# Kernel tuning notes

Measured on AMD Instinct MI355X. Metric: run time of the kernel, lower is better.

## Reference

```python
import jax, jax.numpy as jnp
import numpy as np

INPUT_DIM = 1024
OUTPUT_DIM = 1024
DEGREE = 8
BATCH = 8192


def setup_inputs() -> dict:
    key = jax.random.key(0)
    k1, k2 = jax.random.split(key)
    x = jax.random.normal(k1, (BATCH, INPUT_DIM), dtype=jnp.float32)
    std = 1.0 / (INPUT_DIM * (DEGREE + 1))
    cheby_coeffs = jax.random.normal(k2, (DEGREE + 1, INPUT_DIM, OUTPUT_DIM), dtype=jnp.float32) * std
    tanh_scale = jnp.array(1.0, dtype=jnp.float32)
    tanh_bias = jnp.array(0.0, dtype=jnp.float32)
    return {"x": x, "cheby_coeffs": cheby_coeffs, "tanh_scale": tanh_scale, "tanh_bias": tanh_bias}


def _cheby_basis(x, degree):
    Ts = [jnp.ones_like(x)]
    if degree >= 1:
        Ts.append(x)
    for _ in range(2, degree + 1):
        Ts.append(2.0 * x * Ts[-1] - Ts[-2])
    return jnp.stack(Ts, axis=0)


def reference(x, cheby_coeffs, tanh_scale, tanh_bias):
    degree = cheby_coeffs.shape[0] - 1
    input_dim = cheby_coeffs.shape[1]
    xf = x.reshape(-1, input_dim)
    xt = jnp.tanh(xf * tanh_scale + tanh_bias)            # (B, I)
    cheby = _cheby_basis(xt, degree)                       # (D+1, B, I)
    # bmm over degree then sum over degree == single contraction
    y = jnp.einsum('dbi,dio->bo', cheby, cheby_coeffs)     # (B, O)
    return y
```

## Files before the change

### kernel.cpp

```cpp
#include <hip/hip_runtime.h>
#include <hip/hip_bf16.h>

typedef __attribute__((ext_vector_type(8))) short short8;
typedef __attribute__((ext_vector_type(4))) float f32x4;
typedef __attribute__((ext_vector_type(16))) float f32x16;

#define WS_B0_OFFSET  18874368u

__global__ void wt2_kernel(const float* __restrict__ W, short* __restrict__ Wt2) {
    int bid = blockIdx.x;
    int d = bid >> 7, q = bid & 127;
    int t = threadIdx.x;
    const float* src = W + (size_t)d * 1048576 + (size_t)q * 8 * 1024;
    short* dst = Wt2 + ((size_t)(d * 128 + q) << 13);
#pragma unroll
    for (int u = 0; u < 4; u++) {
        int o = u * 256 + t;
        short8 v;
#pragma unroll
        for (int j = 0; j < 8; j++)
            v[j] = (short)__bfloat16_as_ushort(__float2bfloat16(src[(size_t)j * 1024 + o]));
        *(short8*)(dst + (size_t)o * 8) = v;
    }
}

__global__ void colsum1(const float* __restrict__ W, float* __restrict__ part) {
    int s = blockIdx.x >> 2;
    int o = (blockIdx.x & 3) * 256 + threadIdx.x;
    const float* p = W + (size_t)s * 32 * 1024 + o;
    float acc = 0.f;
#pragma unroll
    for (int i = 0; i < 32; i++) acc += p[(size_t)i * 1024];
    part[s * 1024 + o] = acc;
}
__global__ void colsum2(const float* __restrict__ part, float* __restrict__ b0) {
    int o = blockIdx.x * 256 + threadIdx.x;
    float acc = 0.f;
#pragma unroll
    for (int s = 0; s < 32; s++) acc += part[s * 1024 + o];
    b0[o] = acc;
}

__device__ __forceinline__ float fast_tanh(float t) {
    float e = __expf(t + t);
    return 1.0f - 2.0f * __builtin_amdgcn_rcpf(e + 1.0f);
}

extern "C" __global__ void __launch_bounds__(512, 2)
cheby_gemm(const float* __restrict__ x, const short* __restrict__ Wt2,
           const float* __restrict__ b0v, const float* __restrict__ scp,
           const float* __restrict__ bip, float* __restrict__ out) {
    __shared__ __align__(16) char lds[49152];

    const int tid = threadIdx.x, lane = tid & 63, wid = tid >> 6;
    const int wc = wid & 3, kh = wid >> 2;
    const int tn = blockIdx.x & 3, tm = blockIdx.x >> 2;
    const int m0 = tm << 7, n0 = tn << 8;
    const float sc = scp[0], bi = bip[0];
    const char* wtb = (const char*)Wt2;

    const int arow = tid >> 2, ac = tid & 3;
    const int wbyte0 = ac * 2048 + ((arow ^ (ac << 1)) << 4);
    const float* xptr = x + (size_t)(m0 + arow) * 1024 + ac * 8;

    const int cfr = kh * 2 + (lane >> 5);
    const int abase = cfr * 2048 + (((lane & 31) ^ (cfr << 1)) << 4);
    int bofs[2];
#pragma unroll
    for (int n = 0; n < 2; n++)
        bofs[n] = cfr * 16384 + (n0 + wc * 64 + n * 32 + (lane & 31)) * 16;

    auto bld = [&](short8* bf, int dd, int icc) {
        const char* p = wtb + ((size_t)(dd * 128 + icc * 4) << 14);
#pragma unroll
        for (int n = 0; n < 2; n++)
            bf[n] = *(const short8*)(p + bofs[n]);
    };

    f32x4 xv0, xv1;
    auto loadx = [&](int icc) {
        const float* p = xptr + (icc << 5);
        xv0 = *(const f32x4*)p;
        xv1 = *(const f32x4*)(p + 4);
    };

    float x2[8], tA[8], tB[8];
    auto dotanh = [&]() {
#pragma unroll
        for (int j = 0; j < 4; j++) {
            tA[j]     = fast_tanh(fmaf(xv0[j], sc, bi));
            tA[j + 4] = fast_tanh(fmaf(xv1[j], sc, bi));
        }
#pragma unroll
        for (int j = 0; j < 8; j++) x2[j] = tA[j] + tA[j];
    };
    auto writeA = [&](const float* t, int wbuf) {
        short8 v;
#pragma unroll
        for (int j = 0; j < 8; j++)
            v[j] = (short)__bfloat16_as_ushort(__float2bfloat16(t[j]));
        *(short8*)(lds + wbuf * 8192 + wbyte0) = v;
    };
    auto readA = [&](short8* af, int buf) {
#pragma unroll
        for (int m = 0; m < 4; m++)
            af[m] = *(const short8*)(lds + buf * 8192 + abase + m * 512);
    };

    f32x16 acc[4][2];
#pragma unroll
    for (int n = 0; n < 2; n++) {
        float v = (kh == 0) ? b0v[n0 + wc * 64 + n * 32 + (lane & 31)] : 0.0f;
        f32x16 a;
#pragma unroll
        for (int r = 0; r < 16; r++) a[r] = v;
#pragma unroll
        for (int m = 0; m < 4; m++) acc[m][n] = a;
    }

    auto domfma = [&](const short8* af, const short8* bf) {
        __builtin_amdgcn_s_setprio(1);
#pragma unroll
        for (int m = 0; m < 4; m++)
#pragma unroll
            for (int n = 0; n < 2; n++)
                acc[m][n] = __builtin_amdgcn_mfma_f32_32x32x16_bf16(af[m], bf[n], acc[m][n], 0, 0, 0);
        __builtin_amdgcn_s_setprio(0);
    };

    short8 af0[4], af1[4], bfA[2], bfB[2];

#define DRAIN_BAR                                                 \
    __builtin_amdgcn_sched_barrier(0);                            \
    asm volatile("s_waitcnt lgkmcnt(0)" ::: "memory");            \
    __builtin_amdgcn_s_barrier();

    loadx(0);
    bld(bfA, 1, 0);
    dotanh();
    writeA(tA, 0);
    DRAIN_BAR
    readA(af0, 0);
    __builtin_amdgcn_sched_barrier(0);

#define RSTEP(AFU, AFP, BFU, BFL, LD, LIC, WB, RECUR, XPRE)       \
    {                                                             \
        domfma(AFU, BFU);                                         \
        __builtin_amdgcn_sched_barrier(0);                        \
        bld(BFL, LD, LIC);                                        \
        if (XPRE) loadx(icn);                                     \
        RECUR                                                     \
        DRAIN_BAR                                                 \
        readA(AFP, WB);                                           \
        __builtin_amdgcn_sched_barrier(0);                        \
    }
#define REC_T2  { for (int j = 0; j < 8; j++) tB[j] = fmaf(x2[j], tA[j], -1.0f);  writeA(tB, 1); }
#define REC_BA(WB) { for (int j = 0; j < 8; j++) tA[j] = fmaf(x2[j], tB[j], -tA[j]); writeA(tA, WB); }
#define REC_AB(WB) { for (int j = 0; j < 8; j++) tB[j] = fmaf(x2[j], tA[j], -tB[j]); writeA(tB, WB); }
#define REC_TANH { dotanh(); writeA(tA, 0); }

    for (int ic = 0; ic < 32; ++ic) {
        const int icn = ic < 31 ? ic + 1 : 31;
        RSTEP(af0, af1, bfA, bfB, 2, ic, 1, REC_T2,     0)
        RSTEP(af1, af0, bfB, bfA, 3, ic, 0, REC_BA(0),  0)
        RSTEP(af0, af1, bfA, bfB, 4, ic, 1, REC_AB(1),  0)
        RSTEP(af1, af0, bfB, bfA, 5, ic, 0, REC_BA(0),  0)
        RSTEP(af0, af1, bfA, bfB, 6, ic, 1, REC_AB(1),  0)
        RSTEP(af1, af0, bfB, bfA, 7, ic, 0, REC_BA(0),  1)
        RSTEP(af0, af1, bfA, bfB, 8, ic, 1, REC_AB(1),  0)
        RSTEP(af1, af0, bfB, bfA, 1, icn, 0, REC_TANH,  0)
    }
#undef RSTEP
#undef DRAIN_BAR

#pragma unroll
    for (int m = 0; m < 4; m++) {
        if (kh == 1) {
#pragma unroll
            for (int n = 0; n < 2; n++) {
                char* base = lds + 16384 + (wc * 2 + n) * 4096 + lane * 64;
#pragma unroll
                for (int q = 0; q < 4; q++) {
                    f32x4 v = {acc[m][n][q * 4 + 0], acc[m][n][q * 4 + 1],
                               acc[m][n][q * 4 + 2], acc[m][n][q * 4 + 3]};
                    *(f32x4*)(base + ((q ^ (lane & 3)) << 4)) = v;
                }
            }
        }
        __syncthreads();
        if (kh == 0) {
#pragma unroll
            for (int n = 0; n < 2; n++) {
                const char* base = lds + 16384 + (wc * 2 + n) * 4096 + lane * 64;
#pragma unroll
                for (int q = 0; q < 4; q++) {
                    f32x4 v = *(const f32x4*)(base + ((q ^ (lane & 3)) << 4));
#pragma unroll
                    for (int e = 0; e < 4; e++) acc[m][n][q * 4 + e] += v[e];
                }
            }
        }
        __syncthreads();
    }

    if (kh == 0) {
#pragma unroll
        for (int m = 0; m < 4; m++) {
            int rbase = m0 + m * 32 + ((lane >> 5) << 2);
#pragma unroll
            for (int n = 0; n < 2; n++) {
                int colg = n0 + wc * 64 + n * 32 + (lane & 31);
#pragma unroll
                for (int r = 0; r < 16; r++) {
                    int rowg = rbase + (r & 3) + 8 * (r >> 2);
                    out[(size_t)rowg * 1024 + colg] = acc[m][n][r];
                }
            }
        }
    }
}

extern "C" void kernel_launch(void* const* d_in, const int* in_sizes, int n_in,
                              void* d_out, int out_size, void* d_ws, size_t ws_size,
                              hipStream_t stream) {
    const float* x  = (const float*)d_in[0];
    const float* W  = (const float*)d_in[1];
    const float* sc = (const float*)d_in[2];
    const float* bi = (const float*)d_in[3];
    float* out = (float*)d_out;

    short* Wt2 = (short*)d_ws;
    float* b0  = (float*)((char*)d_ws + WS_B0_OFFSET);
    float* part = out;

    hipLaunchKernelGGL(wt2_kernel, dim3(9 * 128), dim3(256), 0, stream, W, Wt2);
    hipLaunchKernelGGL(colsum1, dim3(128), dim3(256), 0, stream, W, part);
    hipLaunchKernelGGL(colsum2, dim3(4), dim3(256), 0, stream, part, b0);
    hipLaunchKernelGGL(cheby_gemm, dim3(256), dim3(512), 0, stream, x, Wt2, b0, sc, bi, out);
}
```

Measured before the change: 166.9 us.

## Process two Chebyshev degrees per barrier region with four-buffer LDS ring

Restructures the main loop so each barrier-separated region handles two degrees: it reads two A tiles from LDS, issues two MFMA bursts, prefetches two B fragments and computes two recurrence steps before a single barrier. The LDS A buffer grows from two to four slots (48KB to 64KB total) and the reduction scratch moves up accordingly. This halves the number of workgroup barriers and lgkm drains per K chunk. The cost is more live registers (four B fragment sets plus two A sets) and more LDS, which may pressure the two-blocks-per-CU occupancy target.

```diff
diff --git a/kernel.cpp b/kernel.cpp
--- a/kernel.cpp
+++ b/kernel.cpp
@@ -50,7 +50,7 @@
 cheby_gemm(const float* __restrict__ x, const short* __restrict__ Wt2,
            const float* __restrict__ b0v, const float* __restrict__ scp,
            const float* __restrict__ bip, float* __restrict__ out) {
-    __shared__ __align__(16) char lds[49152];
+    __shared__ __align__(16) char lds[65536];
 
     const int tid = threadIdx.x, lane = tid & 63, wid = tid >> 6;
     const int wc = wid & 3, kh = wid >> 2;
@@ -101,11 +101,6 @@
             v[j] = (short)__bfloat16_as_ushort(__float2bfloat16(t[j]));
         *(short8*)(lds + wbuf * 8192 + wbyte0) = v;
     };
-    auto readA = [&](short8* af, int buf) {
-#pragma unroll
-        for (int m = 0; m < 4; m++)
-            af[m] = *(const short8*)(lds + buf * 8192 + abase + m * 512);
-    };
 
     f32x16 acc[4][2];
 #pragma unroll
@@ -118,7 +113,7 @@
         for (int m = 0; m < 4; m++) acc[m][n] = a;
     }
 
-    auto domfma = [&](const short8* af, const short8* bf) {
+    auto burst = [&](const short8* af, const short8* bf) {
         __builtin_amdgcn_s_setprio(1);
 #pragma unroll
         for (int m = 0; m < 4; m++)
@@ -128,49 +123,66 @@
         __builtin_amdgcn_s_setprio(0);
     };
 
-    short8 af0[4], af1[4], bfA[2], bfB[2];
+    short8 bf0[2], bf1[2], bf2[2], bf3[2];
 
 #define DRAIN_BAR                                                 \
     __builtin_amdgcn_sched_barrier(0);                            \
     asm volatile("s_waitcnt lgkmcnt(0)" ::: "memory");            \
-    __builtin_amdgcn_s_barrier();
+    __builtin_amdgcn_s_barrier();                                 \
+    __builtin_amdgcn_sched_barrier(0);
+
+#define REGION(RA, RB, BU0, BU1, BL0, BL1, LD0, LD1, LIC, XPRE, RECUR)  \
+    {                                                                   \
+        short8 afa[4], afb[4];                                          \
+_Pragma("unroll")                                                       \
+        for (int m = 0; m < 4; m++)                                     \
+            afa[m] = *(const short8*)(lds + (RA) * 8192 + abase + m * 512); \
+        burst(afa, BU0);                                                \
+_Pragma("unroll")                                                       \
+        for (int m = 0; m < 4; m++)                                     \
+            afb[m] = *(const short8*)(lds + (RB) * 8192 + abase + m * 512); \
+        burst(afb, BU1);                                                \
+        bld(BL0, LD0, LIC); bld(BL1, LD1, LIC);                         \
+        if (XPRE) loadx(icn);                                           \
+        RECUR                                                           \
+        DRAIN_BAR                                                       \
+    }
+#define REC_STD(WA, WB)                                                 \
+    {                                                                   \
+_Pragma("unroll")                                                       \
+        for (int j = 0; j < 8; j++) tA[j] = fmaf(x2[j], tB[j], -tA[j]); \
+        writeA(tA, WA);                                                 \
+_Pragma("unroll")                                                       \
+        for (int j = 0; j < 8; j++) tB[j] = fmaf(x2[j], tA[j], -tB[j]); \
+        writeA(tB, WB);                                                 \
+    }
+#define REC_TANH(WA, WB)                                                \
+    {                                                                   \
+        dotanh();                                                       \
+_Pragma("unroll")                                                       \
+        for (int j = 0; j < 8; j++) tB[j] = fmaf(x2[j], tA[j], -1.0f);  \
+        writeA(tA, WA);                                                 \
+        writeA(tB, WB);                                                 \
+    }
 
     loadx(0);
-    bld(bfA, 1, 0);
+    bld(bf0, 1, 0); bld(bf1, 2, 0);
     dotanh();
-    writeA(tA, 0);
+#pragma unroll
+    for (int j = 0; j < 8; j++) tB[j] = fmaf(x2[j], tA[j], -1.0f);
+    writeA(tA, 1); writeA(tB, 2);
     DRAIN_BAR
-    readA(af0, 0);
-    __builtin_amdgcn_sched_barrier(0);
-
-#define RSTEP(AFU, AFP, BFU, BFL, LD, LIC, WB, RECUR, XPRE)       \
-    {                                                             \
-        domfma(AFU, BFU);                                         \
-        __builtin_amdgcn_sched_barrier(0);                        \
-        bld(BFL, LD, LIC);                                        \
-        if (XPRE) loadx(icn);                                     \
-        RECUR                                                     \
-        DRAIN_BAR                                                 \
-        readA(AFP, WB);                                           \
-        __builtin_amdgcn_sched_barrier(0);                        \
-    }
-#define REC_T2  { for (int j = 0; j < 8; j++) tB[j] = fmaf(x2[j], tA[j], -1.0f);  writeA(tB, 1); }
-#define REC_BA(WB) { for (int j = 0; j < 8; j++) tA[j] = fmaf(x2[j], tB[j], -tA[j]); writeA(tA, WB); }
-#define REC_AB(WB) { for (int j = 0; j < 8; j++) tB[j] = fmaf(x2[j], tA[j], -tB[j]); writeA(tB, WB); }
-#define REC_TANH { dotanh(); writeA(tA, 0); }
 
     for (int ic = 0; ic < 32; ++ic) {
         const int icn = ic < 31 ? ic + 1 : 31;
-        RSTEP(af0, af1, bfA, bfB, 2, ic, 1, REC_T2,     0)
-        RSTEP(af1, af0, bfB, bfA, 3, ic, 0, REC_BA(0),  0)
-        RSTEP(af0, af1, bfA, bfB, 4, ic, 1, REC_AB(1),  0)
-        RSTEP(af1, af0, bfB, bfA, 5, ic, 0, REC_BA(0),  0)
-        RSTEP(af0, af1, bfA, bfB, 6, ic, 1, REC_AB(1),  0)
-        RSTEP(af1, af0, bfB, bfA, 7, ic, 0, REC_BA(0),  1)
-        RSTEP(af0, af1, bfA, bfB, 8, ic, 1, REC_AB(1),  0)
-        RSTEP(af1, af0, bfB, bfA, 1, icn, 0, REC_TANH,  0)
-    }
-#undef RSTEP
+        REGION(1, 2, bf0, bf1, bf2, bf3, 3, 4, ic,  0, REC_STD(3, 0))
+        REGION(3, 0, bf2, bf3, bf0, bf1, 5, 6, ic,  0, REC_STD(1, 2))
+        REGION(1, 2, bf0, bf1, bf2, bf3, 7, 8, ic,  1, REC_STD(3, 0))
+        REGION(3, 0, bf2, bf3, bf0, bf1, 1, 2, icn, 0, REC_TANH(1, 2))
+    }
+#undef REGION
+#undef REC_STD
+#undef REC_TANH
 #undef DRAIN_BAR
 
 #pragma unroll
@@ -178,7 +190,7 @@
         if (kh == 1) {
 #pragma unroll
             for (int n = 0; n < 2; n++) {
-                char* base = lds + 16384 + (wc * 2 + n) * 4096 + lane * 64;
+                char* base = lds + 32768 + (wc * 2 + n) * 4096 + lane * 64;
 #pragma unroll
                 for (int q = 0; q < 4; q++) {
                     f32x4 v = {acc[m][n][q * 4 + 0], acc[m][n][q * 4 + 1],
@@ -191,7 +203,7 @@
         if (kh == 0) {
 #pragma unroll
             for (int n = 0; n < 2; n++) {
-                const char* base = lds + 16384 + (wc * 2 + n) * 4096 + lane * 64;
+                const char* base = lds + 32768 + (wc * 2 + n) * 4096 + lane * 64;
 #pragma unroll
                 for (int q = 0; q < 4; q++) {
                     f32x4 v = *(const f32x4*)(base + ((q ^ (lane & 3)) << 4));
```

Result: faster. 151.2 us (-9.4%).

## Reshape warp tile to 64x128 and move A reads into each step

Applied to the files above, without the earlier changes.

Warps within each K-half now form a 2x2 grid, each owning a 64-row by 128-column tile, where before each owned the full 128 rows by 64 columns. This halves the A-fragment LDS reads per warp and doubles the global B fragment loads per warp, so shared-memory traffic goes down while global/L2 load volume goes up. The per-step schedule is also reordered: A fragments are read from LDS at the start of each step alongside the next B prefetch, then the MFMA burst runs before the barrier. This removes the separate af0/af1 double-buffer registers, but each step's MFMAs now wait on their own LDS reads.

```diff
diff --git a/kernel.cpp b/kernel.cpp
--- a/kernel.cpp
+++ b/kernel.cpp
@@ -53,7 +53,7 @@
     __shared__ __align__(16) char lds[49152];
 
     const int tid = threadIdx.x, lane = tid & 63, wid = tid >> 6;
-    const int wc = wid & 3, kh = wid >> 2;
+    const int wr = wid & 1, wc = (wid >> 1) & 1, kh = wid >> 2;
     const int tn = blockIdx.x & 3, tm = blockIdx.x >> 2;
     const int m0 = tm << 7, n0 = tn << 8;
     const float sc = scp[0], bi = bip[0];
@@ -64,16 +64,16 @@
     const float* xptr = x + (size_t)(m0 + arow) * 1024 + ac * 8;
 
     const int cfr = kh * 2 + (lane >> 5);
-    const int abase = cfr * 2048 + (((lane & 31) ^ (cfr << 1)) << 4);
-    int bofs[2];
-#pragma unroll
-    for (int n = 0; n < 2; n++)
-        bofs[n] = cfr * 16384 + (n0 + wc * 64 + n * 32 + (lane & 31)) * 16;
+    const int abase = cfr * 2048 + (((lane & 31) ^ (cfr << 1)) << 4) + wr * 1024;
+    int bofs[4];
+#pragma unroll
+    for (int n = 0; n < 4; n++)
+        bofs[n] = (cfr << 14) + ((n0 + wc * 128 + n * 32 + (lane & 31)) << 4);
 
     auto bld = [&](short8* bf, int dd, int icc) {
         const char* p = wtb + ((size_t)(dd * 128 + icc * 4) << 14);
 #pragma unroll
-        for (int n = 0; n < 2; n++)
+        for (int n = 0; n < 4; n++)
             bf[n] = *(const short8*)(p + bofs[n]);
     };
 
@@ -101,119 +101,122 @@
             v[j] = (short)__bfloat16_as_ushort(__float2bfloat16(t[j]));
         *(short8*)(lds + wbuf * 8192 + wbyte0) = v;
     };
-    auto readA = [&](short8* af, int buf) {
-#pragma unroll
-        for (int m = 0; m < 4; m++)
-            af[m] = *(const short8*)(lds + buf * 8192 + abase + m * 512);
-    };
-
-    f32x16 acc[4][2];
-#pragma unroll
-    for (int n = 0; n < 2; n++) {
-        float v = (kh == 0) ? b0v[n0 + wc * 64 + n * 32 + (lane & 31)] : 0.0f;
+
+    f32x16 acc[2][4];
+#pragma unroll
+    for (int n = 0; n < 4; n++) {
+        float v = (kh == 0) ? b0v[n0 + wc * 128 + n * 32 + (lane & 31)] : 0.0f;
         f32x16 a;
 #pragma unroll
         for (int r = 0; r < 16; r++) a[r] = v;
-#pragma unroll
-        for (int m = 0; m < 4; m++) acc[m][n] = a;
-    }
-
-    auto domfma = [&](const short8* af, const short8* bf) {
+        acc[0][n] = a;
+        acc[1][n] = a;
+    }
+
+    auto burst = [&](const short8* af, const short8* bf) {
         __builtin_amdgcn_s_setprio(1);
 #pragma unroll
-        for (int m = 0; m < 4; m++)
-#pragma unroll
-            for (int n = 0; n < 2; n++)
+        for (int m = 0; m < 2; m++)
+#pragma unroll
+            for (int n = 0; n < 4; n++)
                 acc[m][n] = __builtin_amdgcn_mfma_f32_32x32x16_bf16(af[m], bf[n], acc[m][n], 0, 0, 0);
         __builtin_amdgcn_s_setprio(0);
     };
 
-    short8 af0[4], af1[4], bfA[2], bfB[2];
+    short8 bfs[2][4];
 
 #define DRAIN_BAR                                                 \
     __builtin_amdgcn_sched_barrier(0);                            \
     asm volatile("s_waitcnt lgkmcnt(0)" ::: "memory");            \
-    __builtin_amdgcn_s_barrier();
+    __builtin_amdgcn_s_barrier();                                 \
+    __builtin_amdgcn_sched_barrier(0);
+
+#define STEP(S, LD, LIC, RECUR, XPRE)                             \
+    {                                                             \
+        short8 af[2];                                             \
+_Pragma("unroll")                                                 \
+        for (int mm = 0; mm < 2; mm++)                            \
+            af[mm] = *(const short8*)(lds + ((S) & 1) * 8192 + abase + mm * 512); \
+        bld(bfs[((S) + 1) & 1], LD, LIC);                         \
+        if (XPRE) loadx(icn);                                     \
+        RECUR                                                     \
+        burst(af, bfs[(S) & 1]);                                  \
+        DRAIN_BAR                                                 \
+    }
+#define REC_T2   { for (int j = 0; j < 8; j++) tB[j] = fmaf(x2[j], tA[j], -1.0f);  writeA(tB, 1); }
+#define REC_A(WB){ for (int j = 0; j < 8; j++) tA[j] = fmaf(x2[j], tB[j], -tA[j]); writeA(tA, WB); }
+#define REC_B(WB){ for (int j = 0; j < 8; j++) tB[j] = fmaf(x2[j], tA[j], -tB[j]); writeA(tB, WB); }
+#define REC_TANH { dotanh(); writeA(tA, 0); }
 
     loadx(0);
-    bld(bfA, 1, 0);
+    bld(bfs[0], 1, 0);
     dotanh();
     writeA(tA, 0);
     DRAIN_BAR
-    readA(af0, 0);
-    __builtin_amdgcn_sched_barrier(0);
-
-#define RSTEP(AFU, AFP, BFU, BFL, LD, LIC, WB, RECUR, XPRE)       \
-    {                                                             \
-        domfma(AFU, BFU);                                         \
-        __builtin_amdgcn_sched_barrier(0);                        \
-        bld(BFL, LD, LIC);                                        \
-        if (XPRE) loadx(icn);                                     \
-        RECUR                                                     \
-        DRAIN_BAR                                                 \
-        readA(AFP, WB);                                           \
-        __builtin_amdgcn_sched_barrier(0);                        \
-    }
-#define REC_T2  { for (int j = 0; j < 8; j++) tB[j] = fmaf(x2[j], tA[j], -1.0f);  writeA(tB, 1); }
-#define REC_BA(WB) { for (int j = 0; j < 8; j++) tA[j] = fmaf(x2[j], tB[j], -tA[j]); writeA(tA, WB); }
-#define REC_AB(WB) { for (int j = 0; j < 8; j++) tB[j] = fmaf(x2[j], tA[j], -tB[j]); writeA(tB, WB); }
-#define REC_TANH { dotanh(); writeA(tA, 0); }
 
     for (int ic = 0; ic < 32; ++ic) {
         const int icn = ic < 31 ? ic + 1 : 31;
-        RSTEP(af0, af1, bfA, bfB, 2, ic, 1, REC_T2,     0)
-        RSTEP(af1, af0, bfB, bfA, 3, ic, 0, REC_BA(0),  0)
-        RSTEP(af0, af1, bfA, bfB, 4, ic, 1, REC_AB(1),  0)
-        RSTEP(af1, af0, bfB, bfA, 5, ic, 0, REC_BA(0),  0)
-        RSTEP(af0, af1, bfA, bfB, 6, ic, 1, REC_AB(1),  0)
-        RSTEP(af1, af0, bfB, bfA, 7, ic, 0, REC_BA(0),  1)
-        RSTEP(af0, af1, bfA, bfB, 8, ic, 1, REC_AB(1),  0)
-        RSTEP(af1, af0, bfB, bfA, 1, icn, 0, REC_TANH,  0)
-    }
-#undef RSTEP
+        STEP(0, 2, ic,  REC_T2,   0)
+        STEP(1, 3, ic,  REC_A(0), 0)
+        STEP(2, 4, ic,  REC_B(1), 0)
+        STEP(3, 5, ic,  REC_A(0), 0)
+        STEP(4, 6, ic,  REC_B(1), 0)
+        STEP(5, 7, ic,  REC_A(0), 1)
+        STEP(6, 8, ic,  REC_B(1), 0)
+        STEP(7, 1, icn, REC_TANH, 0)
+    }
+#undef STEP
+#undef REC_T2
+#undef REC_A
+#undef REC_B
+#undef REC_TANH
 #undef DRAIN_BAR
 
 #pragma unroll
-    for (int m = 0; m < 4; m++) {
-        if (kh == 1) {
-#pragma unroll
-            for (int n = 0; n < 2; n++) {
-                char* base = lds + 16384 + (wc * 2 + n) * 4096 + lane * 64;
-#pragma unroll
-                for (int q = 0; q < 4; q++) {
-                    f32x4 v = {acc[m][n][q * 4 + 0], acc[m][n][q * 4 + 1],
-                               acc[m][n][q * 4 + 2], acc[m][n][q * 4 + 3]};
-                    *(f32x4*)(base + ((q ^ (lane & 3)) << 4)) = v;
+    for (int mm = 0; mm < 2; mm++)
+#pragma unroll
+        for (int np = 0; np < 2; np++) {
+            if (kh == 1) {
+#pragma unroll
+                for (int nn = 0; nn < 2; nn++) {
+                    int n = np * 2 + nn;
+                    char* base = lds + 16384 + (((wr * 2 + wc) * 2 + nn) << 12) + lane * 64;
+#pragma unroll
+                    for (int q = 0; q < 4; q++) {
+                        f32x4 v = {acc[mm][n][q * 4 + 0], acc[mm][n][q * 4 + 1],
+                                   acc[mm][n][q * 4 + 2], acc[mm][n][q * 4 + 3]};
+                        *(f32x4*)(base + ((q ^ (lane & 3)) << 4)) = v;
+                    }
                 }
             }
-        }
-        __syncthreads();
-        if (kh == 0) {
-#pragma unroll
-            for (int n = 0; n < 2; n++) {
-                const char* base = lds + 16384 + (wc * 2 + n) * 4096 + lane * 64;
-#pragma unroll
-                for (int q = 0; q < 4; q++) {
-                    f32x4 v = *(const f32x4*)(base + ((q ^ (lane & 3)) << 4));
-#pragma unroll
-                    for (int e = 0; e < 4; e++) acc[m][n][q * 4 + e] += v[e];
+            __syncthreads();
+            if (kh == 0) {
+#pragma unroll
+                for (int nn = 0; nn < 2; nn++) {
+                    int n = np * 2 + nn;
+                    const char* base = lds + 16384 + (((wr * 2 + wc) * 2 + nn) << 12) + lane * 64;
+#pragma unroll
+                    for (int q = 0; q < 4; q++) {
+                        f32x4 v = *(const f32x4*)(base + ((q ^ (lane & 3)) << 4));
+#pragma unroll
+                        for (int e = 0; e < 4; e++) acc[mm][n][q * 4 + e] += v[e];
+                    }
                 }
             }
+            __syncthreads();
         }
-        __syncthreads();
-    }
 
     if (kh == 0) {
 #pragma unroll
-        for (int m = 0; m < 4; m++) {
-            int rbase = m0 + m * 32 + ((lane >> 5) << 2);
-#pragma unroll
-            for (int n = 0; n < 2; n++) {
-                int colg = n0 + wc * 64 + n * 32 + (lane & 31);
+        for (int mm = 0; mm < 2; mm++) {
+            int rbase = m0 + wr * 64 + mm * 32 + ((lane >> 5) << 2);
+#pragma unroll
+            for (int n = 0; n < 4; n++) {
+                int colg = n0 + wc * 128 + n * 32 + (lane & 31);
 #pragma unroll
                 for (int r = 0; r < 16; r++) {
                     int rowg = rbase + (r & 3) + 8 * (r >> 2);
-                    out[(size_t)rowg * 1024 + colg] = acc[m][n][r];
+                    out[(size_t)rowg * 1024 + colg] = acc[mm][n][r];
                 }
             }
         }
```

After: 159.1 us. 1.05x faster.
